# Optimization experiments

Hardware: AMD Instinct MI355X
Metric: run time of the kernel (lower is better)

The kernel has to match this reference:

```python
import jax, jax.numpy as jnp
import numpy as np

B = 8192
FL = 96      # feature_len
K = 3        # dynamic filter kernel size
NOUT = 2
EPS = 1e-5
P = (K - 1) // 2

def _lrelu(x):
    return jnp.where(x >= 0, x, 0.1 * x)

def _conv1d(x, w, b):
    # x: [b,1,L], w: [1,1,3], b: [1]; padding=1, stride=1
    y = jax.lax.conv_general_dilated(x, w, (1,), [(1, 1)], dimension_numbers=('NCH', 'OIH', 'NCH'))
    return y + b[None, :, None]

def _bn(y, g, be, m, v):
    # eval-mode BatchNorm1d with running stats
    return (y - m) / jnp.sqrt(v + EPS) * g + be


def setup_inputs() -> dict:
    key = jax.random.key(0)
    ks = jax.random.split(key, 40)
    d = {'x': jax.random.normal(ks[0], (B, 576), jnp.float32)}
    # trans_layer: 6 conv1d (1->1, k=3)
    for i in range(6):
        d[f'cw{i+1}'] = jax.random.normal(ks[1 + i], (1, 1, 3), jnp.float32) * 0.4
        d[f'cb{i+1}'] = jax.random.normal(ks[7 + i], (1,), jnp.float32) * 0.1
    # fusion_layer.de_dimen: Linear(FL -> K*K)
    d['de_W'] = jax.random.normal(ks[13], (K * K, FL), jnp.float32) * 0.1
    d['de_b'] = jnp.zeros((K * K,), jnp.float32)
    # reshape_layer: Linear(2*FL -> 3*FL) + BN
    d['rs_W'] = jax.random.normal(ks[14], (3 * FL, 2 * FL), jnp.float32) * 0.07
    d['rs_b'] = jnp.zeros((3 * FL,), jnp.float32)
    d['rs_g'] = 1.0 + 0.1 * jax.random.normal(ks[15], (3 * FL,), jnp.float32)
    d['rs_be'] = 0.1 * jax.random.normal(ks[16], (3 * FL,), jnp.float32)
    d['rs_m'] = 0.05 * jax.random.normal(ks[17], (3 * FL,), jnp.float32)
    d['rs_v'] = jax.random.uniform(ks[18], (3 * FL,), jnp.float32, 0.5, 1.5)
    # classifier_shallow: Linear(6*FL -> 3*FL) + BN + ReLU + Linear(3*FL -> NOUT)
    d['cl_W1'] = jax.random.normal(ks[19], (3 * FL, 6 * FL), jnp.float32) * 0.05
    d['cl_b1'] = jnp.zeros((3 * FL,), jnp.float32)
    d['cl_g'] = 1.0 + 0.1 * jax.random.normal(ks[20], (3 * FL,), jnp.float32)
    d['cl_be'] = 0.1 * jax.random.normal(ks[21], (3 * FL,), jnp.float32)
    d['cl_m'] = 0.05 * jax.random.normal(ks[22], (3 * FL,), jnp.float32)
    d['cl_v'] = jax.random.uniform(ks[23], (3 * FL,), jnp.float32, 0.5, 1.5)
    d['cl_W2'] = jax.random.normal(ks[24], (NOUT, 3 * FL), jnp.float32) * 0.05
    d['cl_b2'] = jnp.zeros((NOUT,), jnp.float32)
    return d


def reference(x, cw1, cb1, cw2, cb2, cw3, cb3, cw4, cb4, cw5, cb5, cw6, cb6,
              de_W, de_b, rs_W, rs_b, rs_g, rs_be, rs_m, rs_v,
              cl_W1, cl_b1, cl_g, cl_be, cl_m, cl_v, cl_W2, cl_b2):
    def trans(c):  # c: [b,1,3*FL] -> three [b,1,FL]
        s1, s2, s3 = c[..., :FL], c[..., FL:2 * FL], c[..., 2 * FL:]
        x1 = _lrelu(_conv1d(s1, cw1, cb1))
        x2 = _lrelu(_conv1d(s2, cw2, cb2))
        x3 = _lrelu(_conv1d(s3, cw3, cb3))
        return (_lrelu(_conv1d(x1, cw4, cb4)),
                _lrelu(_conv1d(x2, cw5, cb5)),
                _lrelu(_conv1d(x3, cw6, cb6)))

    def fusion(arm, x86, bert):  # each [b,1,FL]
        b = arm.shape[0]
        # c==1 so matmul(s_1^T, s_2) is a per-sample outer product: [b,FL,FL]
        m = _lrelu(jnp.einsum('bl,bm->blm', arm[:, 0], x86[:, 0]))
        # per-sample 3x3 dynamic filter from bert embedding
        s3 = _lrelu(bert[:, 0] @ de_W.T + de_b).reshape(b, 1, K, K)
        fe = jax.lax.conv_general_dilated(
            m.reshape(1, b, FL, FL), s3, (1, 1), [(P, P), (P, P)],
            feature_group_count=b, dimension_numbers=('NCHW', 'OIHW', 'NCHW'))
        fe = _lrelu(fe).reshape(b, FL, FL)
        # AvgPool1d(FL) == mean over last dim (and over rows for the permuted map)
        return jnp.concatenate([fe.mean(axis=2), fe.mean(axis=1)], axis=1)  # [b,2*FL]

    def resh(e):
        return _lrelu(_bn(e @ rs_W.T + rs_b, rs_g, rs_be, rs_m, rs_v))

    xu = x[:, None, :]  # unsqueeze(dim=1)
    c1, c2 = xu[..., :3 * FL], xu[..., 3 * FL:]
    e1 = resh(fusion(*trans(c1))) + c1[:, 0]
    e2 = resh(fusion(*trans(c2))) + c2[:, 0]
    ce = jnp.concatenate([e1, e2], axis=1)  # [b,6*FL]
    # Dropout is identity in eval mode
    h = jax.nn.relu(_bn(ce @ cl_W1.T + cl_b1, cl_g, cl_be, cl_m, cl_v))
    return h @ cl_W2.T + cl_b2  # [b,NOUT]
```

## Files before the change

### kernel.cpp

```cpp
#include <hip/hip_runtime.h>
#include <hip/hip_bf16.h>
#include <math.h>

#define FLn 96
#define SEG 288
#define EPRE_DIM 192
#define EPS_BN 1e-5f

typedef __attribute__((ext_vector_type(8))) short short8;
typedef __attribute__((ext_vector_type(4))) float floatx4;

__device__ __forceinline__ float lrelu(float v) { return fmaxf(v, 0.1f * v); }
__device__ __forceinline__ short f2bf(float f) {
  __hip_bfloat16 h = __float2bfloat16(f);
  return *reinterpret_cast<short*>(&h);
}

__global__ __launch_bounds__(256) void k0_cast(
    const float* __restrict__ rsW, const float* __restrict__ clW1,
    __hip_bfloat16* __restrict__ wB2, __hip_bfloat16* __restrict__ wB3) {
  int idx = blockIdx.x * 256 + threadIdx.x;
  int stride = gridDim.x * 256;
  for (int i = idx; i < 288 * 192; i += stride) wB2[i] = __float2bfloat16(rsW[i]);
  for (int i = idx; i < 288 * 576; i += stride) wB3[i] = __float2bfloat16(clW1[i]);
}

#define O_CIN 0
#define O_ST1 288
#define O_APP 576
#define O_ANP 674
#define O_XPP 772
#define O_XNP 870
#define O_BERT 968
#define O_WKER 1064
#define O_ABF 1088
#define O_BBF 1472
#define O_RP 0
#define SLICE 2048

__global__ __launch_bounds__(256) void k1_persample(
    const float* __restrict__ x,
    const float* __restrict__ cw1, const float* __restrict__ cb1,
    const float* __restrict__ cw2, const float* __restrict__ cb2,
    const float* __restrict__ cw3, const float* __restrict__ cb3,
    const float* __restrict__ cw4, const float* __restrict__ cb4,
    const float* __restrict__ cw5, const float* __restrict__ cb5,
    const float* __restrict__ cw6, const float* __restrict__ cb6,
    const float* __restrict__ deW, const float* __restrict__ deb,
    __hip_bfloat16* __restrict__ epre) {
  __shared__ float sl[4 * SLICE];
  const int tid = threadIdx.x;
  const int wave = tid >> 6;
  const int lane = tid & 63;
  const int quad = lane >> 4;
  const int l16 = lane & 15;
  const int unit = blockIdx.x * 4 + wave;
  float* S = sl + wave * SLICE;
  short* Ssh = (short*)S;
  const float* xrow = x + (size_t)(unit >> 1) * 576 + (unit & 1) * 288;

  const float a0w0 = cw1[0], a0w1 = cw1[1], a0w2 = cw1[2], a0b = cb1[0];
  const float a1w0 = cw2[0], a1w1 = cw2[1], a1w2 = cw2[2], a1b = cb2[0];
  const float a2w0 = cw3[0], a2w1 = cw3[1], a2w2 = cw3[2], a2b = cb3[0];
  const float b0w0 = cw4[0], b0w1 = cw4[1], b0w2 = cw4[2], b0b = cb4[0];
  const float b1w0 = cw5[0], b1w1 = cw5[1], b1w2 = cw5[2], b1b = cb5[0];
  const float b2w0 = cw6[0], b2w1 = cw6[1], b2w2 = cw6[2], b2b = cb6[0];

  for (int t4 = lane; t4 < 72; t4 += 64)
    *(float4*)&S[O_CIN + 4 * t4] = ((const float4*)xrow)[t4];
  if (lane < 8) S[576 + 98 * (lane >> 1) + (lane & 1) * 97] = 0.f;

  for (int t = lane; t < SEG; t += 64) {
    bool g1 = t >= 96, g2 = t >= 192;
    float wa = g2 ? a2w0 : (g1 ? a1w0 : a0w0);
    float wb = g2 ? a2w1 : (g1 ? a1w1 : a0w1);
    float wc = g2 ? a2w2 : (g1 ? a1w2 : a0w2);
    float bb = g2 ? a2b  : (g1 ? a1b  : a0b);
    int p = t - (g2 ? 192 : (g1 ? 96 : 0));
    float l = p > 0 ? S[O_CIN + t - 1] : 0.f;
    float m = S[O_CIN + t];
    float r = p < FLn - 1 ? S[O_CIN + t + 1] : 0.f;
    S[O_ST1 + t] = lrelu(fmaf(wa, l, fmaf(wb, m, fmaf(wc, r, bb))));
  }
  for (int t = lane; t < SEG; t += 64) {
    bool g1 = t >= 96, g2 = t >= 192;
    float wa = g2 ? b2w0 : (g1 ? b1w0 : b0w0);
    float wb = g2 ? b2w1 : (g1 ? b1w1 : b0w1);
    float wc = g2 ? b2w2 : (g1 ? b1w2 : b0w2);
    float bb = g2 ? b2b  : (g1 ? b1b  : b0b);
    int p = t - (g2 ? 192 : (g1 ? 96 : 0));
    float l = p > 0 ? S[O_ST1 + t - 1] : 0.f;
    float m = S[O_ST1 + t];
    float r = p < FLn - 1 ? S[O_ST1 + t + 1] : 0.f;
    float v = lrelu(fmaf(wa, l, fmaf(wb, m, fmaf(wc, r, bb))));
    if (!g1) {
      S[O_APP + 1 + p] = fmaxf(v, 0.1f * v);
      S[O_ANP + 1 + p] = fminf(v, 0.1f * v);
    } else if (!g2) {
      S[O_XPP + 1 + p] = fmaxf(v, 0.f);
      S[O_XNP + 1 + p] = fminf(v, 0.f);
    } else {
      S[O_BERT + p] = v;
    }
  }
  if (quad < 3) {
    float bv[6];
#pragma unroll
    for (int k = 0; k < 6; ++k) bv[k] = S[O_BERT + l16 + 16 * k];
#pragma unroll
    for (int oi = 0; oi < 3; ++oi) {
      int o = quad * 3 + oi;
      float p = 0.f;
#pragma unroll
      for (int k = 0; k < 6; ++k) p = fmaf(bv[k], deW[o * 96 + l16 + 16 * k], p);
      p += __shfl_xor(p, 1, 16);
      p += __shfl_xor(p, 2, 16);
      p += __shfl_xor(p, 4, 16);
      p += __shfl_xor(p, 8, 16);
      if (l16 == 0) S[O_WKER + o] = lrelu(p + deb[o]);
    }
  }
  float w9[9];
#pragma unroll
  for (int q = 0; q < 9; ++q) w9[q] = S[O_WKER + q];

  for (int t = lane; t < 96; t += 64) {
    float xp0 = S[O_XPP + t], xp1 = S[O_XPP + t + 1], xp2 = S[O_XPP + t + 2];
    float xn0 = S[O_XNP + t], xn1 = S[O_XNP + t + 1], xn2 = S[O_XNP + t + 2];
    short8 b;
#pragma unroll
    for (int d = 0; d < 3; ++d) {
      float cp = fmaf(w9[3 * d], xp0, fmaf(w9[3 * d + 1], xp1, w9[3 * d + 2] * xp2));
      float cn = fmaf(w9[3 * d], xn0, fmaf(w9[3 * d + 1], xn1, w9[3 * d + 2] * xn2));
      b[d] = f2bf(cp);
      b[3 + d] = f2bf(cn);
    }
    b[6] = 0; b[7] = 0;
    *(short8*)&Ssh[2 * O_BBF + t * 8] = b;
  }
  for (int m = lane; m < 96; m += 64) {
    short8 a;
    a[0] = f2bf(S[O_APP + m]);
    a[1] = f2bf(S[O_APP + m + 1]);
    a[2] = f2bf(S[O_APP + m + 2]);
    a[3] = f2bf(S[O_ANP + m]);
    a[4] = f2bf(S[O_ANP + m + 1]);
    a[5] = f2bf(S[O_ANP + m + 2]);
    a[6] = 0; a[7] = 0;
    *(short8*)&Ssh[2 * O_ABF + m * 8] = a;
  }

  short8 aF[6];
#pragma unroll
  for (int mt = 0; mt < 6; ++mt) {
    short8 t = *(const short8*)&Ssh[2 * O_ABF + (mt * 16 + l16) * 8];
#pragma unroll
    for (int j = 0; j < 8; ++j) aF[mt][j] = (quad == 0) ? t[j] : (short)0;
  }

  float rowpart[6][4];
#pragma unroll
  for (int mt = 0; mt < 6; ++mt)
#pragma unroll
    for (int r = 0; r < 4; ++r) rowpart[mt][r] = 0.f;
  float cs[6];
#pragma unroll
  for (int s = 0; s < 6; ++s) cs[s] = 0.f;

#pragma unroll
  for (int s = 0; s < 6; ++s) {
    short8 tb = *(const short8*)&Ssh[2 * O_BBF + (s * 16 + l16) * 8];
    short8 bF;
#pragma unroll
    for (int j = 0; j < 8; ++j) bF[j] = (quad == 0) ? tb[j] : (short)0;
    floatx4 accv[6];
#pragma unroll
    for (int mt = 0; mt < 6; ++mt)
      accv[mt] = __builtin_amdgcn_mfma_f32_16x16x32_bf16(
          aF[mt], bF, (floatx4){0.f, 0.f, 0.f, 0.f}, 0, 0, 0);
#pragma unroll
    for (int mt = 0; mt < 6; ++mt) {
#pragma unroll
      for (int r = 0; r < 4; ++r) {
        float sv = accv[mt][r];
        float f = fmaxf(sv, 0.1f * sv);
        rowpart[mt][r] += f;
        cs[s] += f;
      }
    }
  }

#pragma unroll
  for (int mt = 0; mt < 6; ++mt)
    *(float4*)&S[O_RP + (quad * 6 + mt) * 68 + l16 * 4] =
        make_float4(rowpart[mt][0], rowpart[mt][1], rowpart[mt][2], rowpart[mt][3]);
  for (int i = lane; i < 96; i += 64) {
    int g = ((i >> 2) & 3) * 6 + (i >> 4);
    int r = i & 3;
    float s = 0.f;
#pragma unroll
    for (int l = 0; l < 16; ++l) s += S[O_RP + g * 68 + l * 4 + r];
    epre[(size_t)unit * EPRE_DIM + i] = __float2bfloat16(s * (1.f / FLn));
  }
#pragma unroll
  for (int s = 0; s < 6; ++s) {
    float v = cs[s];
    v += __shfl_xor(v, 16, 64);
    v += __shfl_xor(v, 32, 64);
    if (quad == 0)
      epre[(size_t)unit * EPRE_DIM + FLn + s * 16 + l16] =
          __float2bfloat16(v * (1.f / FLn));
  }
}

template <int AS, int KTOT, int MODE>
__global__ __launch_bounds__(256) void gemm_mfma(
    const short* __restrict__ A, const short* __restrict__ W,
    const float* __restrict__ bb, const float* __restrict__ gg,
    const float* __restrict__ be, const float* __restrict__ mm,
    const float* __restrict__ vv,
    const float* __restrict__ resid, __hip_bfloat16* __restrict__ out) {
  __shared__ short sA[128 * 40];
  __shared__ short sB[32 * 40];
  const int tid = threadIdx.x;
  const int lane = tid & 63;
  const int w = tid >> 6;
  const int quad = lane >> 4;
  const int l16 = lane & 15;
  const int row0 = (blockIdx.x / 9) * 128;
  const int out0 = (blockIdx.x % 9) * 32;

  floatx4 acc[2][2];
#pragma unroll
  for (int mi = 0; mi < 2; ++mi)
#pragma unroll
    for (int ni = 0; ni < 2; ++ni) acc[mi][ni] = (floatx4){0.f, 0.f, 0.f, 0.f};

  const int ar = tid >> 1;
  const int ah = tid & 1;
  for (int kc = 0; kc < KTOT; kc += 32) {
    {
      const float4* src = (const float4*)&A[(size_t)(row0 + ar) * AS + kc + ah * 16];
      float4 v0 = src[0];
      float4 v1 = src[1];
      *(float4*)&sA[ar * 40 + ah * 16] = v0;
      *(float4*)&sA[ar * 40 + ah * 16 + 8] = v1;
      if (tid < 64) {
        const float4* bs = (const float4*)&W[(size_t)(out0 + ar) * KTOT + kc + ah * 16];
        float4 u0 = bs[0];
        float4 u1 = bs[1];
        *(float4*)&sB[ar * 40 + ah * 16] = u0;
        *(float4*)&sB[ar * 40 + ah * 16 + 8] = u1;
      }
    }
    __syncthreads();
    short8 aF0 = *(const short8*)&sA[(w * 32 + l16) * 40 + quad * 8];
    short8 aF1 = *(const short8*)&sA[(w * 32 + 16 + l16) * 40 + quad * 8];
    short8 bF0 = *(const short8*)&sB[l16 * 40 + quad * 8];
    short8 bF1 = *(const short8*)&sB[(16 + l16) * 40 + quad * 8];
    acc[0][0] = __builtin_amdgcn_mfma_f32_16x16x32_bf16(aF0, bF0, acc[0][0], 0, 0, 0);
    acc[0][1] = __builtin_amdgcn_mfma_f32_16x16x32_bf16(aF0, bF1, acc[0][1], 0, 0, 0);
    acc[1][0] = __builtin_amdgcn_mfma_f32_16x16x32_bf16(aF1, bF0, acc[1][0], 0, 0, 0);
    acc[1][1] = __builtin_amdgcn_mfma_f32_16x16x32_bf16(aF1, bF1, acc[1][1], 0, 0, 0);
    __syncthreads();
  }

#pragma unroll
  for (int ni = 0; ni < 2; ++ni) {
    const int n_g = out0 + ni * 16 + l16;
    const float vb = bb[n_g];
    const float sc = gg[n_g] * rsqrtf(vv[n_g] + EPS_BN);
    const float mu = mm[n_g];
    const float vbe = be[n_g];
#pragma unroll
    for (int mi = 0; mi < 2; ++mi) {
#pragma unroll
      for (int r = 0; r < 4; ++r) {
        const int m_g = row0 + w * 32 + mi * 16 + quad * 4 + r;
        float y = acc[mi][ni][r] + vb;
        float o = (y - mu) * sc + vbe;
        float val;
        if (MODE == 0) {
          val = lrelu(o) + resid[(size_t)m_g * 288 + n_g];
        } else {
          val = fmaxf(o, 0.f);
        }
        out[(size_t)m_g * 288 + n_g] = __float2bfloat16(val);
      }
    }
  }
}

__global__ __launch_bounds__(256) void k4_out(
    const __hip_bfloat16* __restrict__ h, const float* __restrict__ w2,
    const float* __restrict__ b2, float* __restrict__ out) {
  const int wave = threadIdx.x >> 6;
  const int lane = threadIdx.x & 63;
  const int row = blockIdx.x * 4 + wave;
  const __hip_bfloat16* hr = h + (size_t)row * 288;
  float a0 = 0.f, a1 = 0.f;
#pragma unroll
  for (int i = 0; i < 5; ++i) {
    int k = lane + 64 * i;
    if (k < 288) {
      float hv = __bfloat162float(hr[k]);
      a0 = fmaf(hv, w2[k], a0);
      a1 = fmaf(hv, w2[288 + k], a1);
    }
  }
#pragma unroll
  for (int off = 32; off; off >>= 1) {
    a0 += __shfl_xor(a0, off, 64);
    a1 += __shfl_xor(a1, off, 64);
  }
  if (lane == 0) {
    out[row * 2 + 0] = a0 + b2[0];
    out[row * 2 + 1] = a1 + b2[1];
  }
}

extern "C" void kernel_launch(void* const* d_in, const int* in_sizes, int n_in,
                              void* d_out, int out_size, void* d_ws, size_t ws_size,
                              hipStream_t stream) {
  const float* x   = (const float*)d_in[0];
  const float* cw1 = (const float*)d_in[1];  const float* cb1 = (const float*)d_in[2];
  const float* cw2 = (const float*)d_in[3];  const float* cb2 = (const float*)d_in[4];
  const float* cw3 = (const float*)d_in[5];  const float* cb3 = (const float*)d_in[6];
  const float* cw4 = (const float*)d_in[7];  const float* cb4 = (const float*)d_in[8];
  const float* cw5 = (const float*)d_in[9];  const float* cb5 = (const float*)d_in[10];
  const float* cw6 = (const float*)d_in[11]; const float* cb6 = (const float*)d_in[12];
  const float* deW = (const float*)d_in[13]; const float* deb = (const float*)d_in[14];
  const float* rsW = (const float*)d_in[15]; const float* rsb = (const float*)d_in[16];
  const float* rsg = (const float*)d_in[17]; const float* rsbe = (const float*)d_in[18];
  const float* rsm = (const float*)d_in[19]; const float* rsv = (const float*)d_in[20];
  const float* clW1 = (const float*)d_in[21]; const float* clb1 = (const float*)d_in[22];
  const float* clg = (const float*)d_in[23]; const float* clbe = (const float*)d_in[24];
  const float* clm = (const float*)d_in[25]; const float* clv = (const float*)d_in[26];
  const float* clW2 = (const float*)d_in[27]; const float* clb2 = (const float*)d_in[28];

  short* ws   = (short*)d_ws;
  short* epre = ws;
  short* h    = ws;
  short* ce   = ws + 16384 * 192;
  short* wB2  = ce + 16384 * 288;
  short* wB3  = wB2 + 288 * 192;

  hipLaunchKernelGGL(k0_cast, dim3(128), dim3(256), 0, stream,
                     rsW, clW1, (__hip_bfloat16*)wB2, (__hip_bfloat16*)wB3);
  hipLaunchKernelGGL(k1_persample, dim3(4096), dim3(256), 0, stream, x,
                     cw1, cb1, cw2, cb2, cw3, cb3, cw4, cb4, cw5, cb5, cw6, cb6,
                     deW, deb, (__hip_bfloat16*)epre);
  hipLaunchKernelGGL((gemm_mfma<192, 192, 0>), dim3(128 * 9), dim3(256), 0, stream,
                     epre, wB2, rsb, rsg, rsbe, rsm, rsv, x, (__hip_bfloat16*)ce);
  hipLaunchKernelGGL((gemm_mfma<576, 576, 1>), dim3(64 * 9), dim3(256), 0, stream,
                     ce, wB3, clb1, clg, clbe, clm, clv, (const float*)nullptr,
                     (__hip_bfloat16*)h);
  hipLaunchKernelGGL(k4_out, dim3(2048), dim3(256), 0, stream,
                     (const __hip_bfloat16*)h, clW2, clb2, (float*)d_out);
}
```

Baseline: 216.6 us.

## Fuse reshape GEMM, classifier GEMM and output head into one kernel

Replaces the two tiled MFMA GEMM launches and the final output-head kernel with a single kernel. Each block handles 16 samples (32 fusion units): it computes the reshape layer into an LDS tile, then runs the classifier GEMM with its BN/ReLU and the 2-output projection directly from registers. This removes the global round-trips of the ce and h intermediates and two kernel launches. In exchange, each block reads weight fragments straight from global memory without LDS staging, and only 512 blocks are launched, which may limit reuse of the weight loads and occupancy.

Result: no change. 220.1 us (+1.6%).

```diff
diff --git a/kernel.cpp b/kernel.cpp
--- a/kernel.cpp
+++ b/kernel.cpp
@@ -213,109 +213,114 @@
   }
 }
 
-template <int AS, int KTOT, int MODE>
-__global__ __launch_bounds__(256) void gemm_mfma(
-    const short* __restrict__ A, const short* __restrict__ W,
-    const float* __restrict__ bb, const float* __restrict__ gg,
-    const float* __restrict__ be, const float* __restrict__ mm,
-    const float* __restrict__ vv,
-    const float* __restrict__ resid, __hip_bfloat16* __restrict__ out) {
-  __shared__ short sA[128 * 40];
-  __shared__ short sB[32 * 40];
+__global__ __launch_bounds__(256) void k5_fused_tail(
+    const short* __restrict__ epre, const short* __restrict__ wB2,
+    const short* __restrict__ wB3, const float* __restrict__ x,
+    const float* __restrict__ rsb, const float* __restrict__ rsg,
+    const float* __restrict__ rsbe, const float* __restrict__ rsm,
+    const float* __restrict__ rsv,
+    const float* __restrict__ clb1, const float* __restrict__ clg,
+    const float* __restrict__ clbe, const float* __restrict__ clm,
+    const float* __restrict__ clv,
+    const float* __restrict__ clW2, const float* __restrict__ clb2,
+    float* __restrict__ out) {
+  __shared__ short ceT[16 * 584];
+  __shared__ float scr[128];
   const int tid = threadIdx.x;
+  const int w = tid >> 6;
   const int lane = tid & 63;
-  const int w = tid >> 6;
   const int quad = lane >> 4;
   const int l16 = lane & 15;
-  const int row0 = (blockIdx.x / 9) * 128;
-  const int out0 = (blockIdx.x % 9) * 32;
-
-  floatx4 acc[2][2];
-#pragma unroll
-  for (int mi = 0; mi < 2; ++mi)
-#pragma unroll
-    for (int ni = 0; ni < 2; ++ni) acc[mi][ni] = (floatx4){0.f, 0.f, 0.f, 0.f};
-
-  const int ar = tid >> 1;
-  const int ah = tid & 1;
-  for (int kc = 0; kc < KTOT; kc += 32) {
-    {
-      const float4* src = (const float4*)&A[(size_t)(row0 + ar) * AS + kc + ah * 16];
-      float4 v0 = src[0];
-      float4 v1 = src[1];
-      *(float4*)&sA[ar * 40 + ah * 16] = v0;
-      *(float4*)&sA[ar * 40 + ah * 16 + 8] = v1;
-      if (tid < 64) {
-        const float4* bs = (const float4*)&W[(size_t)(out0 + ar) * KTOT + kc + ah * 16];
-        float4 u0 = bs[0];
-        float4 u1 = bs[1];
-        *(float4*)&sB[ar * 40 + ah * 16] = u0;
-        *(float4*)&sB[ar * 40 + ah * 16 + 8] = u1;
-      }
-    }
-    __syncthreads();
-    short8 aF0 = *(const short8*)&sA[(w * 32 + l16) * 40 + quad * 8];
-    short8 aF1 = *(const short8*)&sA[(w * 32 + 16 + l16) * 40 + quad * 8];
-    short8 bF0 = *(const short8*)&sB[l16 * 40 + quad * 8];
-    short8 bF1 = *(const short8*)&sB[(16 + l16) * 40 + quad * 8];
-    acc[0][0] = __builtin_amdgcn_mfma_f32_16x16x32_bf16(aF0, bF0, acc[0][0], 0, 0, 0);
-    acc[0][1] = __builtin_amdgcn_mfma_f32_16x16x32_bf16(aF0, bF1, acc[0][1], 0, 0, 0);
-    acc[1][0] = __builtin_amdgcn_mfma_f32_16x16x32_bf16(aF1, bF0, acc[1][0], 0, 0, 0);
-    acc[1][1] = __builtin_amdgcn_mfma_f32_16x16x32_bf16(aF1, bF1, acc[1][1], 0, 0, 0);
-    __syncthreads();
-  }
-
-#pragma unroll
-  for (int ni = 0; ni < 2; ++ni) {
-    const int n_g = out0 + ni * 16 + l16;
-    const float vb = bb[n_g];
-    const float sc = gg[n_g] * rsqrtf(vv[n_g] + EPS_BN);
-    const float mu = mm[n_g];
-    const float vbe = be[n_g];
-#pragma unroll
-    for (int mi = 0; mi < 2; ++mi) {
-#pragma unroll
-      for (int r = 0; r < 4; ++r) {
-        const int m_g = row0 + w * 32 + mi * 16 + quad * 4 + r;
-        float y = acc[mi][ni][r] + vb;
-        float o = (y - mu) * sc + vbe;
-        float val;
-        if (MODE == 0) {
-          val = lrelu(o) + resid[(size_t)m_g * 288 + n_g];
-        } else {
-          val = fmaxf(o, 0.f);
-        }
-        out[(size_t)m_g * 288 + n_g] = __float2bfloat16(val);
-      }
-    }
-  }
-}
-
-__global__ __launch_bounds__(256) void k4_out(
-    const __hip_bfloat16* __restrict__ h, const float* __restrict__ w2,
-    const float* __restrict__ b2, float* __restrict__ out) {
-  const int wave = threadIdx.x >> 6;
-  const int lane = threadIdx.x & 63;
-  const int row = blockIdx.x * 4 + wave;
-  const __hip_bfloat16* hr = h + (size_t)row * 288;
-  float a0 = 0.f, a1 = 0.f;
-#pragma unroll
-  for (int i = 0; i < 5; ++i) {
-    int k = lane + 64 * i;
-    if (k < 288) {
-      float hv = __bfloat162float(hr[k]);
-      a0 = fmaf(hv, w2[k], a0);
-      a1 = fmaf(hv, w2[288 + k], a1);
-    }
-  }
-#pragma unroll
-  for (int off = 32; off; off >>= 1) {
-    a0 += __shfl_xor(a0, off, 64);
-    a1 += __shfl_xor(a1, off, 64);
-  }
-  if (lane == 0) {
-    out[row * 2 + 0] = a0 + b2[0];
-    out[row * 2 + 1] = a1 + b2[1];
+  const int u0 = blockIdx.x * 32;
+  const int s0 = blockIdx.x * 16;
+
+  const int mt = w & 1;
+  const int ng = w >> 1;
+  short8 aF[6];
+  {
+    const short* arow = epre + (size_t)(u0 + mt * 16 + l16) * 192 + quad * 8;
+#pragma unroll
+    for (int kf = 0; kf < 6; ++kf) aF[kf] = *(const short8*)(arow + kf * 32);
+  }
+
+#pragma unroll 2
+  for (int j = 0; j < 9; ++j) {
+    const int nf = 2 * j + ng;
+    const int n0 = nf * 16;
+    const short* brow = wB2 + (size_t)(n0 + l16) * 192 + quad * 8;
+    floatx4 acc = (floatx4){0.f, 0.f, 0.f, 0.f};
+#pragma unroll
+    for (int kf = 0; kf < 6; ++kf) {
+      short8 bF = *(const short8*)(brow + kf * 32);
+      acc = __builtin_amdgcn_mfma_f32_16x16x32_bf16(aF[kf], bF, acc, 0, 0, 0);
+    }
+    const int n = n0 + l16;
+    const float sc = rsg[n] * rsqrtf(rsv[n] + EPS_BN);
+    const float vb = rsb[n], mu = rsm[n], vbe = rsbe[n];
+#pragma unroll
+    for (int r = 0; r < 4; ++r) {
+      int um = mt * 16 + quad * 4 + r;
+      int trow = um >> 1;
+      int cc = (um & 1) * 288 + n;
+      float y = acc[r] + vb;
+      float o = (y - mu) * sc + vbe;
+      float e = lrelu(o) + x[(size_t)(s0 + trow) * 576 + cc];
+      ceT[trow * 584 + cc] = f2bf(e);
+    }
+  }
+  __syncthreads();
+
+  short8 cF[18];
+#pragma unroll
+  for (int kf = 0; kf < 18; ++kf)
+    cF[kf] = *(const short8*)&ceT[l16 * 584 + kf * 32 + quad * 8];
+
+  float p0[4], p1[4];
+#pragma unroll
+  for (int r = 0; r < 4; ++r) { p0[r] = 0.f; p1[r] = 0.f; }
+
+  for (int nt = w; nt < 18; nt += 4) {
+    const int n0 = nt * 16;
+    const short* brow = wB3 + (size_t)(n0 + l16) * 576 + quad * 8;
+    floatx4 acc = (floatx4){0.f, 0.f, 0.f, 0.f};
+#pragma unroll
+    for (int kf = 0; kf < 18; ++kf) {
+      short8 bF = *(const short8*)(brow + kf * 32);
+      acc = __builtin_amdgcn_mfma_f32_16x16x32_bf16(cF[kf], bF, acc, 0, 0, 0);
+    }
+    const int n = n0 + l16;
+    const float sc = clg[n] * rsqrtf(clv[n] + EPS_BN);
+    const float vb = clb1[n], mu = clm[n], vbe = clbe[n];
+    const float w2a = clW2[n], w2b = clW2[288 + n];
+#pragma unroll
+    for (int r = 0; r < 4; ++r) {
+      float y = acc[r] + vb;
+      float hh = fmaxf((y - mu) * sc + vbe, 0.f);
+      p0[r] = fmaf(hh, w2a, p0[r]);
+      p1[r] = fmaf(hh, w2b, p1[r]);
+    }
+  }
+#pragma unroll
+  for (int r = 0; r < 4; ++r) {
+#pragma unroll
+    for (int off = 1; off < 16; off <<= 1) {
+      p0[r] += __shfl_xor(p0[r], off, 64);
+      p1[r] += __shfl_xor(p1[r], off, 64);
+    }
+  }
+  if (l16 == 0) {
+#pragma unroll
+    for (int r = 0; r < 4; ++r) {
+      scr[(w * 16 + quad * 4 + r) * 2 + 0] = p0[r];
+      scr[(w * 16 + quad * 4 + r) * 2 + 1] = p1[r];
+    }
+  }
+  __syncthreads();
+  if (tid < 32) {
+    int row = tid >> 1, o = tid & 1;
+    float s = scr[row * 2 + o] + scr[(16 + row) * 2 + o] +
+              scr[(32 + row) * 2 + o] + scr[(48 + row) * 2 + o];
+    out[(size_t)(s0 + row) * 2 + o] = s + clb2[o];
   }
 }
 
@@ -340,9 +345,7 @@
 
   short* ws   = (short*)d_ws;
   short* epre = ws;
-  short* h    = ws;
-  short* ce   = ws + 16384 * 192;
-  short* wB2  = ce + 16384 * 288;
+  short* wB2  = ws + 16384 * 192;
   short* wB3  = wB2 + 288 * 192;
 
   hipLaunchKernelGGL(k0_cast, dim3(128), dim3(256), 0, stream,
@@ -350,11 +353,9 @@
   hipLaunchKernelGGL(k1_persample, dim3(4096), dim3(256), 0, stream, x,
                      cw1, cb1, cw2, cb2, cw3, cb3, cw4, cb4, cw5, cb5, cw6, cb6,
                      deW, deb, (__hip_bfloat16*)epre);
-  hipLaunchKernelGGL((gemm_mfma<192, 192, 0>), dim3(128 * 9), dim3(256), 0, stream,
-                     epre, wB2, rsb, rsg, rsbe, rsm, rsv, x, (__hip_bfloat16*)ce);
-  hipLaunchKernelGGL((gemm_mfma<576, 576, 1>), dim3(64 * 9), dim3(256), 0, stream,
-                     ce, wB3, clb1, clg, clbe, clm, clv, (const float*)nullptr,
-                     (__hip_bfloat16*)h);
-  hipLaunchKernelGGL(k4_out, dim3(2048), dim3(256), 0, stream,
-                     (const __hip_bfloat16*)h, clW2, clb2, (float*)d_out);
-}
+  hipLaunchKernelGGL(k5_fused_tail, dim3(512), dim3(256), 0, stream,
+                     epre, wB2, wB3, x,
+                     rsb, rsg, rsbe, rsm, rsv,
+                     clb1, clg, clbe, clm, clv,
+                     clW2, clb2, (float*)d_out);
+}
```
